# Kernel optimization log

Hardware: AMD Instinct MI355X
Metric: run time of the kernel (lower is better)

## Reference

```python
import jax, jax.numpy as jnp
import numpy as np

N_NODES = 200_000
BATCH = 131_072
D = 128          # memory_dim
E = 64           # edge_feat_dim
T = 64           # time_dim
P = 5            # num_prototypes
LN_EPS = 1e-4


def _xavier(key, shape):
    fan_in, fan_out = shape[-1], shape[-2] if len(shape) > 1 else shape[-1]
    lim = float(np.sqrt(6.0 / (fan_in + fan_out)))
    return jax.random.uniform(key, shape, jnp.float32, -lim, lim)


def _ln(x, g, b):
    mu = x.mean(-1, keepdims=True)
    var = ((x - mu) ** 2).mean(-1, keepdims=True)
    return (x - mu) * jax.lax.rsqrt(var + LN_EPS) * g + b


def setup_inputs() -> dict:
    key = jax.random.key(0)
    ks = jax.random.split(key, 14)
    return {
        "node_ids": jax.random.randint(ks[0], (BATCH,), 0, N_NODES),
        "edge_features": jax.random.normal(ks[1], (BATCH, E), jnp.float32),
        "t": jax.random.uniform(ks[2], (BATCH,), jnp.float32),
        "raw_memory": jax.random.normal(ks[3], (N_NODES, D), jnp.float32) * 0.01,
        "all_prototypes": _xavier(ks[4], (N_NODES, P, D)),
        "proto_ln_g": jnp.ones((D,), jnp.float32),
        "proto_ln_b": jnp.zeros((D,), jnp.float32),
        "time_w": jax.random.normal(ks[5], (T,), jnp.float32),
        "time_b": jnp.zeros((T,), jnp.float32),
        "edge_w": _xavier(ks[6], (D, E)),
        "edge_b": jnp.zeros((D,), jnp.float32),
        "query_w": _xavier(ks[7], (D, D + D + T)),
        "query_b": jnp.zeros((D,), jnp.float32),
        "cell_ln_g": jnp.ones((D,), jnp.float32),
        "cell_ln_b": jnp.zeros((D,), jnp.float32),
        "gate_w": _xavier(ks[8], (1, 2 * D + T)),
        "gate_b": jnp.ones((1,), jnp.float32),
        "temperature": jnp.ones((1,), jnp.float32) * 0.1,
    }


def reference(node_ids, edge_features, t, raw_memory, all_prototypes,
              proto_ln_g, proto_ln_b, time_w, time_b, edge_w, edge_b,
              query_w, query_b, cell_ln_g, cell_ln_b, gate_w, gate_b,
              temperature):
    # gather per-interaction state
    raw = raw_memory[node_ids]                                   # [B, D]
    protos = _ln(all_prototypes[node_ids], proto_ln_g, proto_ln_b)  # [B, P, D]
    # projections / time encoding (TimeEncoder: cos(Linear(t)))
    edge = edge_features @ edge_w.T + edge_b                     # [B, D]
    te = jnp.cos(t[:, None] * time_w[None, :] + time_b)          # [B, T]
    # query
    qi = jnp.concatenate([raw, edge, te], axis=-1)               # [B, 2D+T]
    query = jnp.tanh(_ln(qi @ query_w.T + query_b, cell_ln_g, cell_ln_b))
    # cosine similarity over P prototypes
    qn = query / jnp.clip(jnp.linalg.norm(query, axis=-1, keepdims=True), 1e-6)
    pn = protos / jnp.clip(jnp.linalg.norm(protos, axis=-1, keepdims=True), 1e-6)
    sim = jnp.einsum('bd,bpd->bp', qn, pn)
    sim = jnp.clip(sim, -30.0, 30.0)
    temp = jnp.clip(temperature, 0.05, 2.0)
    sim = sim / (temp + 1e-4)
    attn = jnp.nan_to_num(jax.nn.softmax(sim, axis=-1), nan=0.0, posinf=0.0, neginf=0.0)
    # candidate memory + gate
    cand = jnp.clip(jnp.einsum('bp,bpd->bd', attn, protos), -5.0, 5.0)
    gi = jnp.clip(jnp.concatenate([raw, cand, te], axis=-1), -100.0, 100.0)
    gate = jax.nn.sigmoid(gi @ gate_w.T + gate_b)                # [B, 1]
    upd = (1.0 - gate) * raw + gate * cand
    upd = jnp.clip(_ln(upd, cell_ln_g, cell_ln_b), -10.0, 10.0)
    return upd
```

## Files before the change

### kernel.cpp

```cpp
#include <hip/hip_runtime.h>

#define D 128
#define EDIM 64
#define TDIM 64
#define KTOT 256
#define NP 5
#define LN_EPS 1e-4f
#define WSB_OFF 33024

typedef float v4f __attribute__((ext_vector_type(4)));
typedef float f32x4 __attribute__((ext_vector_type(4)));
typedef short bf16x8 __attribute__((ext_vector_type(8)));

__device__ __forceinline__ float clipf(float x, float lo, float hi) {
    return fminf(fmaxf(x, lo), hi);
}

__device__ __forceinline__ unsigned short bf16rne(float x) {
    unsigned int u = __float_as_uint(x);
    unsigned int r = (u + 0x7fffu + ((u >> 16) & 1u)) >> 16;
    return (unsigned short)r;
}
__device__ __forceinline__ float bf16tof(unsigned short h) {
    return __uint_as_float(((unsigned int)h) << 16);
}

template <int CTRL>
__device__ __forceinline__ float dpp_addstep(float v) {
    int o = __builtin_amdgcn_update_dpp(0, __float_as_int(v), CTRL, 0xF, 0xF, true);
    return v + __int_as_float(o);
}
__device__ __forceinline__ float qred16(float v) {
    v = dpp_addstep<0xB1>(v);
    v = dpp_addstep<0x4E>(v);
    v = dpp_addstep<0x124>(v);
    v = dpp_addstep<0x128>(v);
    return v;
}

__global__ void k0_fold(const float* __restrict__ qw, const float* __restrict__ qb,
                        const float* __restrict__ ew, const float* __restrict__ eb,
                        const float* __restrict__ pg, const float* __restrict__ pb,
                        float* __restrict__ ws) {
    const int d = threadIdx.x;
    const int bk = blockIdx.x;
    float* Wt = ws;
    float* c0 = ws + KTOT * D;
    float* cc = c0 + D;
    if (bk < 128) {
        Wt[bk * D + d] = qw[d * 320 + bk];
    } else if (bk < 192) {
        const int e = bk - 128;
        const float4* qrow = (const float4*)(qw + d * 320 + 128);
        float s = 0.f;
        #pragma unroll
        for (int g = 0; g < 32; ++g) {
            float4 q = qrow[g];
            s = fmaf(q.x, ew[(4 * g + 0) * EDIM + e], s);
            s = fmaf(q.y, ew[(4 * g + 1) * EDIM + e], s);
            s = fmaf(q.z, ew[(4 * g + 2) * EDIM + e], s);
            s = fmaf(q.w, ew[(4 * g + 3) * EDIM + e], s);
        }
        Wt[bk * D + d] = s;
    } else if (bk < 256) {
        Wt[bk * D + d] = qw[d * 320 + 256 + (bk - 192)];
    } else if (bk == 256) {
        const float4* qrow = (const float4*)(qw + d * 320 + 128);
        const float4* eb4 = (const float4*)eb;
        float s = qb[d];
        #pragma unroll
        for (int g = 0; g < 32; ++g) {
            float4 q = qrow[g], e4 = eb4[g];
            s = fmaf(q.x, e4.x, s); s = fmaf(q.y, e4.y, s);
            s = fmaf(q.z, e4.z, s); s = fmaf(q.w, e4.w, s);
        }
        c0[d] = s;
    } else {
        if (d == 0) { float s = 0.f; for (int i = 0; i < D; ++i) s = fmaf(pg[i], pg[i], s); cc[0] = s; }
        if (d == 1) { float s = 0.f; for (int i = 0; i < D; ++i) s = fmaf(pg[i], pb[i], s); cc[1] = s; }
        if (d == 2) { float s = 0.f; for (int i = 0; i < D; ++i) s = fmaf(pb[i], pb[i], s); cc[2] = s; }
    }
}

__global__ void k0b_pack(float* __restrict__ ws) {
    const int kb = blockIdx.x >> 3;
    const int nt = blockIdx.x & 7;
    const int l = threadIdx.x;
    const float* Wt = ws;
    const int col = nt * 16 + (l & 15);
    const int kbase = kb * 32 + (l >> 4) * 8;
    bf16x8 hi, lo;
    #pragma unroll
    for (int j = 0; j < 8; ++j) {
        float x = Wt[(kbase + j) * D + col];
        unsigned short h = bf16rne(x);
        hi[j] = (short)h;
        lo[j] = (short)bf16rne(x - bf16tof(h));
    }
    bf16x8* outp = (bf16x8*)(ws + WSB_OFF);
    outp[((kb * 8 + nt) * 2 + 0) * 64 + l] = hi;
    outp[((kb * 8 + nt) * 2 + 1) * 64 + l] = lo;
}

__global__ __launch_bounds__(256, 2)
void k_fused(const int* __restrict__ nids, const float* __restrict__ ef,
             const float* __restrict__ tarr, const float* __restrict__ raw_mem,
             const float* __restrict__ protos,
             const float* __restrict__ pg, const float* __restrict__ pb,
             const float* __restrict__ tw, const float* __restrict__ tb,
             const float* __restrict__ cg, const float* __restrict__ cb,
             const float* __restrict__ gw, const float* __restrict__ gb,
             const float* __restrict__ temp, const float* __restrict__ ws,
             float* __restrict__ out, int Btot) {
    const int tid = threadIdx.x;
    const int lane = tid & 63;
    const int wave = tid >> 6;
    const int m0 = blockIdx.x * 64 + wave * 16;
    const int col = lane & 15;
    const int kg = lane >> 4;

    const int elemA = min(m0 + col, Btot - 1);
    const int nidA = nids[elemA];
    const float* rawpA = raw_mem + (size_t)nidA * D + kg * 8;
    const float* efpA = ef + (size_t)elemA * EDIM + kg * 8;
    const float tvalA = tarr[elemA];
    const bf16x8* wb = (const bf16x8*)(ws + WSB_OFF);

    f32x4 acc[8];
    #pragma unroll
    for (int nt = 0; nt < 8; ++nt) acc[nt] = (f32x4){0.f, 0.f, 0.f, 0.f};

    #pragma unroll 1
    for (int kb = 0; kb < 8; ++kb) {
        float xs[8];
        if (kb < 4) {
            v4f a = *(const v4f*)(rawpA + kb * 32);
            v4f b = *(const v4f*)(rawpA + kb * 32 + 4);
            xs[0] = a[0]; xs[1] = a[1]; xs[2] = a[2]; xs[3] = a[3];
            xs[4] = b[0]; xs[5] = b[1]; xs[6] = b[2]; xs[7] = b[3];
        } else if (kb < 6) {
            v4f a = *(const v4f*)(efpA + (kb - 4) * 32);
            v4f b = *(const v4f*)(efpA + (kb - 4) * 32 + 4);
            xs[0] = a[0]; xs[1] = a[1]; xs[2] = a[2]; xs[3] = a[3];
            xs[4] = b[0]; xs[5] = b[1]; xs[6] = b[2]; xs[7] = b[3];
        } else {
            const int u0 = (kb - 6) * 32 + kg * 8;
            v4f wa = *(const v4f*)(tw + u0);
            v4f wbv = *(const v4f*)(tw + u0 + 4);
            v4f ba = *(const v4f*)(tb + u0);
            v4f bbv = *(const v4f*)(tb + u0 + 4);
            xs[0] = __cosf(fmaf(tvalA, wa[0], ba[0]));
            xs[1] = __cosf(fmaf(tvalA, wa[1], ba[1]));
            xs[2] = __cosf(fmaf(tvalA, wa[2], ba[2]));
            xs[3] = __cosf(fmaf(tvalA, wa[3], ba[3]));
            xs[4] = __cosf(fmaf(tvalA, wbv[0], bbv[0]));
            xs[5] = __cosf(fmaf(tvalA, wbv[1], bbv[1]));
            xs[6] = __cosf(fmaf(tvalA, wbv[2], bbv[2]));
            xs[7] = __cosf(fmaf(tvalA, wbv[3], bbv[3]));
        }
        bf16x8 ahi, alo;
        #pragma unroll
        for (int j = 0; j < 8; ++j) {
            unsigned short h = bf16rne(xs[j]);
            ahi[j] = (short)h;
            alo[j] = (short)bf16rne(xs[j] - bf16tof(h));
        }
        #pragma unroll
        for (int nt = 0; nt < 8; ++nt) {
            bf16x8 bhi = wb[((kb * 8 + nt) * 2 + 0) * 64 + lane];
            bf16x8 blo = wb[((kb * 8 + nt) * 2 + 1) * 64 + lane];
            acc[nt] = __builtin_amdgcn_mfma_f32_16x16x32_bf16(ahi, bhi, acc[nt], 0, 0, 0);
            acc[nt] = __builtin_amdgcn_mfma_f32_16x16x32_bf16(ahi, blo, acc[nt], 0, 0, 0);
            acc[nt] = __builtin_amdgcn_mfma_f32_16x16x32_bf16(alo, bhi, acc[nt], 0, 0, 0);
        }
    }

    const float* c0 = ws + KTOT * D;
    const float sbb = (ws + KTOT * D + D)[2];
    const float tempc = fminf(fmaxf(temp[0], 0.05f), 2.0f) + 1e-4f;
    const float its = 1.0f / tempc;
    const float gbias = gb[0];

    float pg8[8], pb8[8], cg8[8], cb8[8], gwr8[8], gwc8[8], c08[8];
    #pragma unroll
    for (int j = 0; j < 8; ++j) {
        const int dd = j * 16 + col;
        pg8[j] = pg[dd]; pb8[j] = pb[dd];
        cg8[j] = cg[dd]; cb8[j] = cb[dd];
        gwr8[j] = gw[dd]; gwc8[j] = gw[D + dd];
        c08[j] = c0[dd];
    }
    float twc[4], tbc[4], gwt[4];
    #pragma unroll
    for (int j = 0; j < 4; ++j) {
        const int u = col * 4 + j;
        twc[j] = tw[u]; tbc[j] = tb[u]; gwt[j] = gw[2 * D + u];
    }

    #pragma unroll
    for (int r = 0; r < 4; ++r) {
        const int erow = m0 + kg * 4 + r;
        const bool act = (erow < Btot);
        const int ebb = act ? erow : Btot - 1;
        const int nid = nids[ebb];
        const float* rawrow = raw_mem + (size_t)nid * D;
        const float* prow = protos + (size_t)nid * (NP * D);
        const float tval = tarr[ebb];

        float qv[8], rawv[8];
        #pragma unroll
        for (int j = 0; j < 8; ++j) {
            qv[j] = acc[j][r] + c08[j];
            rawv[j] = rawrow[j * 16 + col];
        }
        float pxv[NP][8];
        #pragma unroll
        for (int p = 0; p < NP; ++p) {
            #pragma unroll
            for (int j = 0; j < 8; ++j) pxv[p][j] = prow[p * D + j * 16 + col];
        }

        float gsum = 0.f;
        #pragma unroll
        for (int j = 0; j < 8; ++j) gsum = fmaf(gwr8[j], clipf(rawv[j], -100.f, 100.f), gsum);
        #pragma unroll
        for (int j = 0; j < 4; ++j) gsum = fmaf(gwt[j], __cosf(fmaf(tval, twc[j], tbc[j])), gsum);

        float sx = 0.f;
        #pragma unroll
        for (int j = 0; j < 8; ++j) sx += qv[j];
        sx = qred16(sx);
        const float mu = sx * (1.f / D);
        float sv = 0.f;
        #pragma unroll
        for (int j = 0; j < 8; ++j) { float a = qv[j] - mu; sv = fmaf(a, a, sv); }
        sv = qred16(sv);
        const float rsq = __builtin_amdgcn_rsqf(sv * (1.f / D) + LN_EPS);

        float ssq = 0.f;
        #pragma unroll
        for (int j = 0; j < 8; ++j) {
            float x = fmaf((qv[j] - mu) * rsq, cg8[j], cb8[j]);
            float e2x = __expf(2.f * x);
            float th = 1.f - 2.f * __builtin_amdgcn_rcpf(e2x + 1.f);
            qv[j] = th;
            ssq = fmaf(th, th, ssq);
        }
        ssq = qred16(ssq);
        const float invq = __builtin_amdgcn_rcpf(fmaxf(sqrtf(ssq), 1e-6f));

        float aqg = 0.f, aqb = 0.f;
        #pragma unroll
        for (int j = 0; j < 8; ++j) {
            float qn = qv[j] * invq;
            float qg = qn * pg8[j];
            aqg += qg;
            aqb = fmaf(qn, pb8[j], aqb);
            qv[j] = qg;
        }
        aqg = qred16(aqg);
        aqb = qred16(aqb);

        float mups[NP], rsps[NP], simv[NP];
        #pragma unroll
        for (int p = 0; p < NP; ++p) {
            float s_x = 0.f, sxx = 0.f, sqgx = 0.f;
            #pragma unroll
            for (int j = 0; j < 8; ++j) {
                float x = pxv[p][j];
                s_x += x;
                sxx = fmaf(x, x, sxx);
                sqgx = fmaf(qv[j], x, sqgx);
            }
            s_x = qred16(s_x); sxx = qred16(sxx); sqgx = qred16(sqgx);
            const float mup = s_x * (1.f / D);
            const float varp = sxx * (1.f / D) - mup * mup;
            const float rsp = __builtin_amdgcn_rsqf(varp + LN_EPS);
            float sz2 = 0.f, szb = 0.f;
            #pragma unroll
            for (int j = 0; j < 8; ++j) {
                float z = (pxv[p][j] - mup) * pg8[j];
                sz2 = fmaf(z, z, sz2);
                szb = fmaf(z, pb8[j], szb);
            }
            sz2 = qred16(sz2); szb = qred16(szb);
            const float dot = fmaf(rsp, sqgx - mup * aqg, aqb);
            float nrm2 = fmaf(rsp * rsp, sz2, fmaf(2.f * rsp, szb, sbb));
            nrm2 = fmaxf(nrm2, 0.f);
            const float inv = __builtin_amdgcn_rcpf(fmaxf(sqrtf(nrm2), 1e-6f));
            mups[p] = mup;
            rsps[p] = rsp;
            simv[p] = clipf(dot * inv, -30.f, 30.f) * its;
        }

        float mx = fmaxf(fmaxf(fmaxf(simv[0], simv[1]), fmaxf(simv[2], simv[3])), simv[4]);
        float wp[NP];
        float Z = 0.f;
        #pragma unroll
        for (int p = 0; p < NP; ++p) { float ev = __expf(simv[p] - mx); wp[p] = ev; Z += ev; }
        const float iZ = 1.f / Z;
        float a0 = 0.f, a1 = 0.f;
        #pragma unroll
        for (int p = 0; p < NP; ++p) {
            float at = wp[p] * iZ;
            a0 += at;
            float w = at * rsps[p];
            a1 = fmaf(w, mups[p], a1);
            wp[p] = w;
        }

        float S8[8];
        #pragma unroll
        for (int j = 0; j < 8; ++j) S8[j] = 0.f;
        #pragma unroll
        for (int p = 0; p < NP; ++p) {
            #pragma unroll
            for (int j = 0; j < 8; ++j) S8[j] = fmaf(wp[p], pxv[p][j], S8[j]);
        }
        float gc = gsum;
        #pragma unroll
        for (int j = 0; j < 8; ++j) {
            float cnd = clipf(fmaf(pg8[j], S8[j] - a1, pb8[j] * a0), -5.f, 5.f);
            gc = fmaf(gwc8[j], cnd, gc);
            S8[j] = cnd;
        }
        gc = qred16(gc);
        const float gpre = gc + gbias;
        const float gate = __builtin_amdgcn_rcpf(1.f + __expf(-gpre));

        float su = 0.f, ssu = 0.f;
        #pragma unroll
        for (int j = 0; j < 8; ++j) {
            float u = fmaf(gate, S8[j] - rawv[j], rawv[j]);
            S8[j] = u;
            su += u;
            ssu = fmaf(u, u, ssu);
        }
        su = qred16(su);
        ssu = qred16(ssu);
        const float muu = su * (1.f / D);
        const float varu = ssu * (1.f / D) - muu * muu;
        const float rsu = __builtin_amdgcn_rsqf(varu + LN_EPS);

        if (act) {
            float* orow = out + (size_t)erow * D;
            #pragma unroll
            for (int j = 0; j < 8; ++j) {
                orow[j * 16 + col] = clipf(fmaf((S8[j] - muu) * rsu, cg8[j], cb8[j]), -10.f, 10.f);
            }
        }
    }
}

extern "C" void kernel_launch(void* const* d_in, const int* in_sizes, int n_in,
                              void* d_out, int out_size, void* d_ws, size_t ws_size,
                              hipStream_t stream) {
    const int*   nids = (const int*)d_in[0];
    const float* ef   = (const float*)d_in[1];
    const float* t    = (const float*)d_in[2];
    const float* raw  = (const float*)d_in[3];
    const float* prot = (const float*)d_in[4];
    const float* pg   = (const float*)d_in[5];
    const float* pb   = (const float*)d_in[6];
    const float* tw   = (const float*)d_in[7];
    const float* tb   = (const float*)d_in[8];
    const float* ew   = (const float*)d_in[9];
    const float* eb   = (const float*)d_in[10];
    const float* qw   = (const float*)d_in[11];
    const float* qb   = (const float*)d_in[12];
    const float* cg   = (const float*)d_in[13];
    const float* cb   = (const float*)d_in[14];
    const float* gw   = (const float*)d_in[15];
    const float* gb   = (const float*)d_in[16];
    const float* temp = (const float*)d_in[17];
    float* ws  = (float*)d_ws;
    float* out = (float*)d_out;
    const int Btot = in_sizes[0];

    hipLaunchKernelGGL(k0_fold, dim3(258), dim3(128), 0, stream,
                       qw, qb, ew, eb, pg, pb, ws);
    hipLaunchKernelGGL(k0b_pack, dim3(64), dim3(64), 0, stream, ws);
    hipLaunchKernelGGL(k_fused, dim3((Btot + 63) / 64), dim3(256), 0, stream,
                       nids, ef, t, raw, prot, pg, pb, tw, tb, cg, cb, gw, gb, temp, ws, out, Btot);
}
```

Baseline: 143.0 us.

## Stage GEMM weights through LDS with register prefetch and raise occupancy

Each k-block's bf16 hi/lo weight tiles are now loaded cooperatively into shared memory, and the next block's weights and activation inputs are prefetched into registers while the MFMAs for the current block run. Gate, time weights and biases move into LDS, and the query bias is folded into the accumulators, which frees registers. Launch bounds go from 2 to 3 blocks per SM. The goal is to hide global load latency and raise occupancy, at the cost of two barriers per k-step and added LDS traffic.

```diff
diff --git a/kernel.cpp b/kernel.cpp
--- a/kernel.cpp
+++ b/kernel.cpp
@@ -102,7 +102,7 @@
     outp[((kb * 8 + nt) * 2 + 1) * 64 + l] = lo;
 }
 
-__global__ __launch_bounds__(256, 2)
+__global__ __launch_bounds__(256, 3)
 void k_fused(const int* __restrict__ nids, const float* __restrict__ ef,
              const float* __restrict__ tarr, const float* __restrict__ raw_mem,
              const float* __restrict__ protos,
@@ -112,6 +112,9 @@
              const float* __restrict__ gw, const float* __restrict__ gb,
              const float* __restrict__ temp, const float* __restrict__ ws,
              float* __restrict__ out, int Btot) {
+    __shared__ bf16x8 Bs[1024];
+    __shared__ float cst[960];
+
     const int tid = threadIdx.x;
     const int lane = tid & 63;
     const int wave = tid >> 6;
@@ -119,82 +122,101 @@
     const int col = lane & 15;
     const int kg = lane >> 4;
 
+    if (tid < 128) {
+        cst[tid] = gw[tid];
+        cst[128 + tid] = gw[128 + tid];
+    } else {
+        const int u = tid - 128;
+        if (u < 64) { cst[256 + u] = tw[u]; cst[320 + u] = tb[u]; }
+        else        { cst[384 + u - 64] = gw[256 + u - 64]; }
+    }
+
     const int elemA = min(m0 + col, Btot - 1);
     const int nidA = nids[elemA];
     const float* rawpA = raw_mem + (size_t)nidA * D + kg * 8;
     const float* efpA = ef + (size_t)elemA * EDIM + kg * 8;
     const float tvalA = tarr[elemA];
-    const bf16x8* wb = (const bf16x8*)(ws + WSB_OFF);
+    const bf16x8* wbg = (const bf16x8*)(ws + WSB_OFF);
 
     f32x4 acc[8];
     #pragma unroll
     for (int nt = 0; nt < 8; ++nt) acc[nt] = (f32x4){0.f, 0.f, 0.f, 0.f};
 
+    bf16x8 s0 = wbg[tid], s1 = wbg[256 + tid], s2 = wbg[512 + tid], s3 = wbg[768 + tid];
+    v4f xa0 = *(const v4f*)rawpA;
+    v4f xa1 = *(const v4f*)(rawpA + 4);
+
     #pragma unroll 1
     for (int kb = 0; kb < 8; ++kb) {
-        float xs[8];
-        if (kb < 4) {
-            v4f a = *(const v4f*)(rawpA + kb * 32);
-            v4f b = *(const v4f*)(rawpA + kb * 32 + 4);
-            xs[0] = a[0]; xs[1] = a[1]; xs[2] = a[2]; xs[3] = a[3];
-            xs[4] = b[0]; xs[5] = b[1]; xs[6] = b[2]; xs[7] = b[3];
-        } else if (kb < 6) {
-            v4f a = *(const v4f*)(efpA + (kb - 4) * 32);
-            v4f b = *(const v4f*)(efpA + (kb - 4) * 32 + 4);
-            xs[0] = a[0]; xs[1] = a[1]; xs[2] = a[2]; xs[3] = a[3];
-            xs[4] = b[0]; xs[5] = b[1]; xs[6] = b[2]; xs[7] = b[3];
-        } else {
-            const int u0 = (kb - 6) * 32 + kg * 8;
-            v4f wa = *(const v4f*)(tw + u0);
-            v4f wbv = *(const v4f*)(tw + u0 + 4);
-            v4f ba = *(const v4f*)(tb + u0);
-            v4f bbv = *(const v4f*)(tb + u0 + 4);
-            xs[0] = __cosf(fmaf(tvalA, wa[0], ba[0]));
-            xs[1] = __cosf(fmaf(tvalA, wa[1], ba[1]));
-            xs[2] = __cosf(fmaf(tvalA, wa[2], ba[2]));
-            xs[3] = __cosf(fmaf(tvalA, wa[3], ba[3]));
-            xs[4] = __cosf(fmaf(tvalA, wbv[0], bbv[0]));
-            xs[5] = __cosf(fmaf(tvalA, wbv[1], bbv[1]));
-            xs[6] = __cosf(fmaf(tvalA, wbv[2], bbv[2]));
-            xs[7] = __cosf(fmaf(tvalA, wbv[3], bbv[3]));
+        __syncthreads();
+        Bs[tid] = s0; Bs[256 + tid] = s1; Bs[512 + tid] = s2; Bs[768 + tid] = s3;
+        __syncthreads();
+        v4f xn0 = xa0, xn1 = xa1;
+        if (kb < 7) {
+            const int kn = kb + 1;
+            const bf16x8* wn = wbg + kn * 1024;
+            s0 = wn[tid]; s1 = wn[256 + tid]; s2 = wn[512 + tid]; s3 = wn[768 + tid];
+            if (kn < 4) {
+                xn0 = *(const v4f*)(rawpA + kn * 32);
+                xn1 = *(const v4f*)(rawpA + kn * 32 + 4);
+            } else if (kn < 6) {
+                xn0 = *(const v4f*)(efpA + (kn - 4) * 32);
+                xn1 = *(const v4f*)(efpA + (kn - 4) * 32 + 4);
+            } else {
+                const int u0 = (kn - 6) * 32 + kg * 8;
+                v4f wa = *(const v4f*)(tw + u0);
+                v4f wb2 = *(const v4f*)(tw + u0 + 4);
+                v4f ba = *(const v4f*)(tb + u0);
+                v4f bb2 = *(const v4f*)(tb + u0 + 4);
+                #pragma unroll
+                for (int j = 0; j < 4; ++j) xn0[j] = __cosf(fmaf(tvalA, wa[j], ba[j]));
+                #pragma unroll
+                for (int j = 0; j < 4; ++j) xn1[j] = __cosf(fmaf(tvalA, wb2[j], bb2[j]));
+            }
         }
         bf16x8 ahi, alo;
         #pragma unroll
-        for (int j = 0; j < 8; ++j) {
-            unsigned short h = bf16rne(xs[j]);
+        for (int j = 0; j < 4; ++j) {
+            unsigned short h = bf16rne(xa0[j]);
             ahi[j] = (short)h;
-            alo[j] = (short)bf16rne(xs[j] - bf16tof(h));
+            alo[j] = (short)bf16rne(xa0[j] - bf16tof(h));
+        }
+        #pragma unroll
+        for (int j = 0; j < 4; ++j) {
+            unsigned short h = bf16rne(xa1[j]);
+            ahi[4 + j] = (short)h;
+            alo[4 + j] = (short)bf16rne(xa1[j] - bf16tof(h));
         }
         #pragma unroll
         for (int nt = 0; nt < 8; ++nt) {
-            bf16x8 bhi = wb[((kb * 8 + nt) * 2 + 0) * 64 + lane];
-            bf16x8 blo = wb[((kb * 8 + nt) * 2 + 1) * 64 + lane];
+            bf16x8 bhi = Bs[(nt * 2 + 0) * 64 + lane];
+            bf16x8 blo = Bs[(nt * 2 + 1) * 64 + lane];
             acc[nt] = __builtin_amdgcn_mfma_f32_16x16x32_bf16(ahi, bhi, acc[nt], 0, 0, 0);
             acc[nt] = __builtin_amdgcn_mfma_f32_16x16x32_bf16(ahi, blo, acc[nt], 0, 0, 0);
             acc[nt] = __builtin_amdgcn_mfma_f32_16x16x32_bf16(alo, bhi, acc[nt], 0, 0, 0);
         }
-    }
-
-    const float* c0 = ws + KTOT * D;
+        xa0 = xn0; xa1 = xn1;
+    }
+
+    {
+        const float* c0 = ws + KTOT * D;
+        #pragma unroll
+        for (int j = 0; j < 8; ++j) {
+            const float cv = c0[j * 16 + col];
+            acc[j][0] += cv; acc[j][1] += cv; acc[j][2] += cv; acc[j][3] += cv;
+        }
+    }
     const float sbb = (ws + KTOT * D + D)[2];
     const float tempc = fminf(fmaxf(temp[0], 0.05f), 2.0f) + 1e-4f;
     const float its = 1.0f / tempc;
     const float gbias = gb[0];
 
-    float pg8[8], pb8[8], cg8[8], cb8[8], gwr8[8], gwc8[8], c08[8];
+    float pg8[8], pb8[8], cg8[8], cb8[8];
     #pragma unroll
     for (int j = 0; j < 8; ++j) {
         const int dd = j * 16 + col;
         pg8[j] = pg[dd]; pb8[j] = pb[dd];
         cg8[j] = cg[dd]; cb8[j] = cb[dd];
-        gwr8[j] = gw[dd]; gwc8[j] = gw[D + dd];
-        c08[j] = c0[dd];
-    }
-    float twc[4], tbc[4], gwt[4];
-    #pragma unroll
-    for (int j = 0; j < 4; ++j) {
-        const int u = col * 4 + j;
-        twc[j] = tw[u]; tbc[j] = tb[u]; gwt[j] = gw[2 * D + u];
     }
 
     #pragma unroll
@@ -210,7 +232,7 @@
         float qv[8], rawv[8];
         #pragma unroll
         for (int j = 0; j < 8; ++j) {
-            qv[j] = acc[j][r] + c08[j];
+            qv[j] = acc[j][r];
             rawv[j] = rawrow[j * 16 + col];
         }
         float pxv[NP][8];
@@ -222,9 +244,13 @@
 
         float gsum = 0.f;
         #pragma unroll
-        for (int j = 0; j < 8; ++j) gsum = fmaf(gwr8[j], clipf(rawv[j], -100.f, 100.f), gsum);
-        #pragma unroll
-        for (int j = 0; j < 4; ++j) gsum = fmaf(gwt[j], __cosf(fmaf(tval, twc[j], tbc[j])), gsum);
+        for (int j = 0; j < 8; ++j)
+            gsum = fmaf(cst[j * 16 + col], clipf(rawv[j], -100.f, 100.f), gsum);
+        #pragma unroll
+        for (int j = 0; j < 4; ++j) {
+            const int u = col * 4 + j;
+            gsum = fmaf(cst[384 + u], __cosf(fmaf(tval, cst[256 + u], cst[320 + u])), gsum);
+        }
 
         float sx = 0.f;
         #pragma unroll
@@ -321,7 +347,7 @@
         #pragma unroll
         for (int j = 0; j < 8; ++j) {
             float cnd = clipf(fmaf(pg8[j], S8[j] - a1, pb8[j] * a0), -5.f, 5.f);
-            gc = fmaf(gwc8[j], cnd, gc);
+            gc = fmaf(cst[128 + j * 16 + col], cnd, gc);
             S8[j] = cnd;
         }
         gc = qred16(gc);
```

New measurement: 120.5 us. 15.7% less time.
